# Performance work log

Measured on AMD Instinct MI355X. Metric: run time of the kernel, lower is better.

The kernel has to match this reference:

```python
import jax, jax.numpy as jnp
import numpy as np

B, N, RD = 32, 2000, 32
E, H, A = 128, 256, 8
NUM_ACTIONS = N
ACTION_NORM = float(NUM_ACTIONS)


def _mlp2(x, W1, b1, W2, b2):
    return jnp.maximum(x @ W1 + b1, 0.0) @ W2 + b2


def setup_inputs() -> dict:
    key = jax.random.key(0)
    ks = jax.random.split(key, 8)
    s = lambda fan_in: 1.0 / np.sqrt(fan_in)
    return {
        "state": jax.random.normal(ks[0], (B, N, RD), jnp.float32),
        "distance_matrix": jax.random.uniform(ks[1], (N, N), jnp.float32),
        "W_emb1": jax.random.normal(ks[2], (RD, H), jnp.float32) * s(RD),
        "b_emb1": jnp.zeros((H,), jnp.float32),
        "W_emb2": jax.random.normal(ks[3], (H, E), jnp.float32) * s(H),
        "b_emb2": jnp.zeros((E,), jnp.float32),
        "Wq1": jax.random.normal(ks[4], (E + A, H), jnp.float32) * s(E + A),
        "bq1": jnp.zeros((H,), jnp.float32),
        "Wq2": jax.random.normal(ks[5], (H, 1), jnp.float32) * s(H),
        "bq2": jnp.zeros((1,), jnp.float32),
        "fixed_actions": jax.random.randint(ks[6], (3, B), 0, NUM_ACTIONS, jnp.int32),
        "fixed_agent_ids": jnp.arange(3, dtype=jnp.int32),
    }


def reference(state, distance_matrix, W_emb1, b_emb1, W_emb2, b_emb2,
              Wq1, bq1, Wq2, bq2, fixed_actions, fixed_agent_ids):
    # normalized distance -> similarity, row-stochastic
    dm = distance_matrix / distance_matrix.max()
    sim = jnp.exp(-dm)  # scaling = 1 (use_nn_scaling=False)
    sim = sim / sim.sum(-1, keepdims=True)

    enc = _mlp2(state, W_emb1, b_emb1, W_emb2, b_emb2)      # [B,N,E]
    x = jnp.einsum('nm,bme->bne', sim, enc)                 # graph conv mix

    idx_f = jnp.arange(N, dtype=x.dtype)

    def qnet(actions):
        # actions: [B,A] broadcast over node axis -> concat -> MLP -> [B,N]
        act = jnp.broadcast_to(actions[:, None, :], (B, N, A))
        feat = jnp.concatenate([x, act], axis=-1)           # [B,N,E+A]
        return _mlp2(feat, Wq1, bq1, Wq2, bq2)[..., 0]      # [B,N]

    # init actions: -1 everywhere, fixed agents get given action / norm
    actions = jnp.full((B, A), -1.0, dtype=x.dtype)
    actions = actions.at[:, fixed_agent_ids].set(
        fixed_actions.T.astype(x.dtype) / ACTION_NORM)

    # sequential per-agent soft-argmax loop (second torch loop; the first
    # torch loop's q-values are fully overwritten here, so it is dead code)
    q_cols = []
    for agent_id in range(A):
        q = qnet(actions)                                   # [B,N]
        sam = jnp.clip(jax.nn.softmax(q, axis=-1) @ idx_f, 0.0, float(NUM_ACTIONS))
        actions = actions.at[:, agent_id].set(
            jax.lax.stop_gradient(sam / ACTION_NORM))
        q2 = qnet(actions)
        qv = jnp.take_along_axis(q2, sam.astype(jnp.int32)[:, None], axis=-1)[:, 0]
        q_cols.append(qv)

    q_values = jnp.stack(q_cols, axis=1)                    # [B,A]
    chosen = (actions * ACTION_NORM).astype(jnp.int32)      # [B,A]
    return q_values, chosen
```

## Files before the change

### kernel.cpp

```cpp
#include <hip/hip_runtime.h>
#include <cstddef>

#define NB 32
#define NN 2000
#define NRD 32
#define NE 128
#define NH 256
#define NA 8
#define KP8 2048
#define NGP 128
#define H1S 264
#define XT8S 136
#define ACTION_NORM 2000.0f

typedef unsigned short u16;
typedef unsigned char u8;
typedef __bf16 b16x8 __attribute__((ext_vector_type(8)));
typedef float f32x4 __attribute__((ext_vector_type(4)));
typedef const __attribute__((address_space(1))) unsigned int* gptr_t;
typedef __attribute__((address_space(3))) unsigned int* lptr_t;

__device__ inline u16 f2bf(float x) {
    unsigned u = __float_as_uint(x);
    u += 0x7FFFu + ((u >> 16) & 1u);
    return (u16)(u >> 16);
}
__device__ inline float bf2f(u16 h) { return __uint_as_float((unsigned)h << 16); }
__device__ inline u8 f2fp8(float x) {
    return (u8)(__builtin_amdgcn_cvt_pk_fp8_f32(x, x, 0, false) & 0xFF);
}
__device__ inline u16 f2fp8x2(float a, float b) {
    return (u16)(__builtin_amdgcn_cvt_pk_fp8_f32(a, b, 0, false) & 0xFFFF);
}
__device__ inline float fp82f(u8 b) {
    return __builtin_amdgcn_cvt_pk_f32_fp8((unsigned)b, false)[0];
}
__device__ inline int kswz(int m) {
    return (m & ~63) + (((m >> 3) & 3) << 4) + (((m >> 5) & 1) << 3) + (m & 7);
}

#define PREP_STATE (64000 * 32)
#define PREP_W1T   (256 * 32)
#define PREP_W2T   (128 * 256)
#define PREP_WQ1T  (256 * 128)
#define PREP_PAD   (4096 * 48)
#define PREP_TOT   (PREP_STATE + PREP_W1T + PREP_W2T + PREP_WQ1T + PREP_PAD)
#define PREP_BLOCKS (PREP_TOT / 256)
#define MAX_BLOCKS 1024
__global__ __launch_bounds__(256) void k_front(
        const float* __restrict__ state, const float* __restrict__ W1,
        const float* __restrict__ W2, const float* __restrict__ Wq1,
        const float* __restrict__ dm, const int* __restrict__ fa,
        const int* __restrict__ fid,
        u16* __restrict__ state_b, u16* __restrict__ W1t,
        u16* __restrict__ W2t, u8* __restrict__ Wq1f8,
        u8* __restrict__ encb, float* __restrict__ pmax,
        float* __restrict__ actions, float* __restrict__ ap0,
        float2* __restrict__ part0) {
    __shared__ float sh[256];
    const int blk = blockIdx.x, t = threadIdx.x;
    if (blk < PREP_BLOCKS) {
        int i = blk * 256 + t;
        if (i < PREP_STATE) { state_b[i] = f2bf(state[i]); return; }
        i -= PREP_STATE;
        if (i < PREP_W1T) { int h = i >> 5, k = i & 31; W1t[i] = f2bf(W1[k * NH + h]); return; }
        i -= PREP_W1T;
        if (i < PREP_W2T) { int e = i >> 8, h = i & 255; W2t[i] = f2bf(W2[h * NE + e]); return; }
        i -= PREP_W2T;
        if (i < PREP_WQ1T) { int hq = i >> 7, e = i & 127; Wq1f8[i] = f2fp8(Wq1[e * NH + hq]); return; }
        i -= PREP_WQ1T;
        if (i < PREP_PAD) { int eb = i / 48, mm = NN + (i % 48); encb[(size_t)eb * KP8 + kswz(mm)] = 0; }
        return;
    }
    if (blk < PREP_BLOCKS + MAX_BLOCKS) {
        const int bid = blk - PREP_BLOCKS;
        float m = 0.0f;
        for (size_t i = (size_t)bid * 256 + t; i < (size_t)NN * NN; i += (size_t)MAX_BLOCKS * 256)
            m = fmaxf(m, dm[i]);
        sh[t] = m; __syncthreads();
        for (int s = 128; s > 0; s >>= 1) {
            if (t < s) sh[t] = fmaxf(sh[t], sh[t + s]);
            __syncthreads();
        }
        if (t == 0) pmax[bid] = sh[0];
        return;
    }
    const int b = t >> 3, a = t & 7;
    float v = -1.0f;
    for (int j = 0; j < 3; ++j)
        if (fid[j] == a) v = (float)fa[j * NB + b] / ACTION_NORM;
    actions[t] = v;
    sh[t] = v;
    __syncthreads();
    float wq[NA];
#pragma unroll
    for (int aa = 0; aa < NA; ++aa) wq[aa] = Wq1[(size_t)(NE + aa) * NH + t];
    for (int bb = 0; bb < NB; ++bb) {
        float s = 0.0f;
#pragma unroll
        for (int aa = 0; aa < NA; ++aa) s = fmaf(sh[bb * NA + aa], wq[aa], s);
        ap0[bb * NH + t] = s;
    }
    for (int i = t; i < NB * NGP; i += 256) part0[i] = make_float2(0.0f, 0.0f);
}

__global__ __launch_bounds__(512) void k_sim(
        const float* __restrict__ dm, const float* __restrict__ pmax,
        u8* __restrict__ simb, float* __restrict__ inv_rs) {
    __shared__ float shf[512];
    __shared__ u8 srow[KP8];
    const int n = blockIdx.x, t = threadIdx.x;
    float m = fmaxf(pmax[t], pmax[t + 512]);
    shf[t] = m; __syncthreads();
    for (int s = 256; s > 0; s >>= 1) {
        if (t < s) shf[t] = fmaxf(shf[t], shf[t + s]);
        __syncthreads();
    }
    const float inv = 1.0f / shf[0];
    __syncthreads();
    float s = 0.0f;
    for (int mm = t * 2; mm < KP8; mm += 1024) {
        float e0 = 0.0f, e1 = 0.0f;
        if (mm < NN)     { e0 = expf(-dm[(size_t)n * NN + mm] * inv);     s += e0; }
        if (mm + 1 < NN) { e1 = expf(-dm[(size_t)n * NN + mm + 1] * inv); s += e1; }
        *(u16*)(srow + kswz(mm)) = f2fp8x2(e0, e1);
    }
    shf[t] = s; __syncthreads();
    for (int st = 256; st > 0; st >>= 1) {
        if (t < st) shf[t] += shf[t + st];
        __syncthreads();
    }
    if (t == 0) inv_rs[n] = 1.0f / shf[0];
    if (t < 128) *(uint4*)(simb + (size_t)n * KP8 + t * 16) = *(const uint4*)(srow + t * 16);
}

__global__ __launch_bounds__(512) void k_enc(
        const u16* __restrict__ state_b, const u16* __restrict__ W1t,
        const u16* __restrict__ W2t, u8* __restrict__ encb,
        const float* __restrict__ b1, const float* __restrict__ b2) {
    __shared__ u16 stage[20 * 512];
    __shared__ u16 h1t[64 * H1S];
    const int blk = blockIdx.x, tid = threadIdx.x;
    const int w = tid >> 6, l = tid & 63;
    const int lm = l & 15, lq = l >> 4;
    const int gm = blk * 64;

    {
#pragma unroll
        for (int i = 0; i < 3; ++i) {
            const int idx = w * 3 + i;
            if (idx < 20) {
                const u16* gp;
                if (idx < 4) gp = state_b + (size_t)(gm + idx * 16 + lm) * NRD + lq * 8;
                else         gp = W1t + (size_t)((idx - 4) * 16 + lm) * NRD + lq * 8;
                __builtin_amdgcn_global_load_lds((gptr_t)gp, (lptr_t)(stage + idx * 512), 16, 0, 0);
            }
        }
        __syncthreads();
        b16x8 af[4], bf[2];
#pragma unroll
        for (int i = 0; i < 4; ++i) af[i] = *(const b16x8*)(stage + i * 512 + l * 8);
#pragma unroll
        for (int j = 0; j < 2; ++j) bf[j] = *(const b16x8*)(stage + (4 + w * 2 + j) * 512 + l * 8);
        f32x4 acc1[4][2] = {};
#pragma unroll
        for (int i = 0; i < 4; ++i)
#pragma unroll
            for (int j = 0; j < 2; ++j)
                acc1[i][j] = __builtin_amdgcn_mfma_f32_16x16x32_bf16(af[i], bf[j], acc1[i][j], 0, 0, 0);
#pragma unroll
        for (int i = 0; i < 4; ++i)
#pragma unroll
            for (int r = 0; r < 4; ++r) {
                const int row = i * 16 + lq * 4 + r;
#pragma unroll
                for (int j = 0; j < 2; ++j) {
                    const int col = w * 32 + j * 16 + lm;
                    h1t[row * H1S + col] = f2bf(fmaxf(acc1[i][j][r] + b1[col], 0.0f));
                }
            }
    }

    const int wr = w & 3, wc = w >> 2;
    f32x4 acc2[2][2] = {};
    const u16* gpw = W2t + (size_t)(w * 16 + lm) * NH + lq * 8;
    __syncthreads();
    __builtin_amdgcn_global_load_lds((gptr_t)gpw, (lptr_t)(stage + w * 512), 16, 0, 0);
    __syncthreads();
    for (int t = 0; t < 8; ++t) {
        const int cur = t & 1;
        if (t < 7) {
            gpw += 32;
            __builtin_amdgcn_global_load_lds((gptr_t)gpw,
                (lptr_t)(stage + (cur ^ 1) * 4096 + w * 512), 16, 0, 0);
        }
        const u16* base = stage + cur * 4096;
        b16x8 af2[2], bf2[2];
#pragma unroll
        for (int i = 0; i < 2; ++i)
            af2[i] = *(const b16x8*)(base + (wr * 2 + i) * 512 + l * 8);
#pragma unroll
        for (int j = 0; j < 2; ++j)
            bf2[j] = *(const b16x8*)(h1t + (wc * 32 + j * 16 + lm) * H1S + t * 32 + lq * 8);
#pragma unroll
        for (int i = 0; i < 2; ++i)
#pragma unroll
            for (int j = 0; j < 2; ++j)
                acc2[i][j] = __builtin_amdgcn_mfma_f32_16x16x32_bf16(af2[i], bf2[j], acc2[i][j], 0, 0, 0);
        __syncthreads();
    }

    u8* etile = (u8*)stage;
#pragma unroll
    for (int i = 0; i < 2; ++i)
#pragma unroll
        for (int r = 0; r < 4; ++r) {
            const int e = wr * 32 + i * 16 + lq * 4 + r;
            const float bias = b2[e];
#pragma unroll
            for (int j = 0; j < 2; ++j) {
                const int off = wc * 32 + j * 16 + lm;
                etile[e * 64 + off] = f2fp8(acc2[i][j][r] + bias);
            }
        }
    __syncthreads();
#pragma unroll
    for (int u0 = 0; u0 < 2; ++u0) {
        const int u = u0 * 512 + tid;
        const int e = u >> 3, run = u & 7;
        const int rg0 = gm + run * 8;
        const unsigned bb = (unsigned)rg0 / 2000u;
        const unsigned m0 = (unsigned)rg0 - bb * 2000u;
        const int wbyte = (int)(m0 & ~63u) + (int)(((m0 >> 3) & 3u) << 4) + (int)(((m0 >> 5) & 1u) << 3);
        const uint2 v = *(const uint2*)(etile + e * 64 + run * 8);
        *(uint2*)(encb + ((size_t)bb * 128 + e) * KP8 + wbyte) = v;
    }
}

__global__ __launch_bounds__(512) void k_conv_y0(
        const u8* __restrict__ simb, const u8* __restrict__ encb,
        const u8* __restrict__ Wq1f8, const float* __restrict__ inv_rs,
        const float* __restrict__ bq1, const float* __restrict__ ap0,
        const float* __restrict__ Wq2, u8* __restrict__ y0f8,
        float2* __restrict__ part0) {
    __shared__ u8 lds[3 * 16384];
    __shared__ float qsum[64 * 8];
    const int tid = threadIdx.x;
    const int w = tid >> 6, l = tid & 63;
    const int wr = w & 1, wc = w >> 1;
    const int L = blockIdx.x + (int)(blockIdx.y << 4);
    const int g = L & 7, ii = L >> 3;
    const int bx = (g & 1) * 8 + (ii & 7);
    const int by = (g >> 1) * 8 + (ii >> 3);
    const int bm = bx * 128;
    const int bb = by;
    const int lm = l & 15, lq = l >> 4;
    const u8* Bt = encb + (size_t)bb * 128 * KP8;
    typedef long lx2 __attribute__((ext_vector_type(2)));

    f32x4 acc[4][2] = {};

    const u8* gpt[2];
#pragma unroll
    for (int i = 0; i < 2; ++i) {
        const int idx = w * 2 + i;
        if (idx < 8) {
            int row = bm + idx * 16 + lm;
            row = row < NN ? row : NN - 1;
            gpt[i] = simb + (size_t)row * KP8 + lq * 16;
        } else {
            gpt[i] = Bt + (size_t)((idx - 8) * 16 + lm) * KP8 + lq * 16;
        }
    }

    auto STAGE = [&](int kt, int buf) {
#pragma unroll
        for (int i = 0; i < 2; ++i)
            __builtin_amdgcn_global_load_lds((gptr_t)(gpt[i] + kt * 64),
                (lptr_t)(lds + buf * 16384 + (w * 2 + i) * 1024), 16, 0, 0);
    };
    auto COMPUTE = [&](int buf) {
        const u8* curb = lds + buf * 16384;
        const int fo = l * 16;
        lx2 af[4], bf[2];
#pragma unroll
        for (int i = 0; i < 4; ++i)
            af[i] = *(const lx2*)(curb + (wr * 4 + i) * 1024 + fo);
#pragma unroll
        for (int j = 0; j < 2; ++j)
            bf[j] = *(const lx2*)(curb + (8 + wc * 2 + j) * 1024 + fo);
        __builtin_amdgcn_s_setprio(1);
#pragma unroll
        for (int i = 0; i < 4; ++i)
#pragma unroll
            for (int j = 0; j < 2; ++j) {
                acc[i][j] = __builtin_amdgcn_mfma_f32_16x16x32_fp8_fp8(af[i][0], bf[j][0], acc[i][j], 0, 0, 0);
                acc[i][j] = __builtin_amdgcn_mfma_f32_16x16x32_fp8_fp8(af[i][1], bf[j][1], acc[i][j], 0, 0, 0);
            }
        __builtin_amdgcn_s_setprio(0);
    };

#define FENCE() __builtin_amdgcn_sched_barrier(0)
#define WAIT_VM(N) do { FENCE(); asm volatile("s_waitcnt vmcnt(" #N ")" ::: "memory"); FENCE(); } while (0)
#define BARRIER() do { FENCE(); __builtin_amdgcn_s_barrier(); FENCE(); } while (0)

    STAGE(0, 0);
    STAGE(1, 1);
    WAIT_VM(2); BARRIER();
    for (int t = 0; t < 30; ++t) {
        STAGE(t + 2, (t + 2) % 3);
        COMPUTE(t % 3);
        WAIT_VM(2); BARRIER();
    }
    COMPUTE(0);
    WAIT_VM(0); BARRIER();
    COMPUTE(1);
    BARRIER();
#undef WAIT_VM
#undef BARRIER
#undef FENCE

#pragma unroll
    for (int i = 0; i < 4; ++i) {
#pragma unroll
        for (int r = 0; r < 4; ++r) {
            const int row = wr * 64 + i * 16 + lq * 4 + r;
            const int gn = bm + row;
            const float rsv = inv_rs[gn < NN ? gn : NN - 1];
#pragma unroll
            for (int j = 0; j < 2; ++j) {
                const int col = wc * 32 + j * 16 + lm;
                lds[row * XT8S + col] = f2fp8(acc[i][j][r] * rsv);
            }
        }
    }
    __syncthreads();

    const int h0 = w * 32;
    float bq1v[2], apv[2], w2vv[2];
#pragma unroll
    for (int j = 0; j < 2; ++j) {
        const int h = h0 + j * 16 + lm;
        bq1v[j] = bq1[h];
        apv[j] = ap0[bb * NH + h];
        w2vv[j] = Wq2[h];
    }
    float se_tot = 0.0f, sn_tot = 0.0f;

    for (int half = 0; half < 2; ++half) {
        f32x4 acc2[4][2] = {};
#pragma unroll
        for (int ks = 0; ks < 4; ++ks) {
            long bfw[2];
#pragma unroll
            for (int j = 0; j < 2; ++j)
                bfw[j] = *(const long*)(Wq1f8 + (size_t)(h0 + j * 16 + lm) * NE + ks * 32 + lq * 8);
#pragma unroll
            for (int i = 0; i < 4; ++i) {
                const long afx = *(const long*)(lds + (half * 64 + i * 16 + lm) * XT8S + ks * 32 + lq * 8);
#pragma unroll
                for (int j = 0; j < 2; ++j)
                    acc2[i][j] = __builtin_amdgcn_mfma_f32_16x16x32_fp8_fp8(afx, bfw[j], acc2[i][j], 0, 0, 0);
            }
        }
#pragma unroll
        for (int i = 0; i < 4; ++i) {
#pragma unroll
            for (int r = 0; r < 4; ++r) {
                const int rl = i * 16 + lq * 4 + r;
                const int n = bm + half * 64 + rl;
                float q = 0.0f;
#pragma unroll
                for (int j = 0; j < 2; ++j) {
                    const float v = acc2[i][j][r] + bq1v[j];
                    if (n < NN) y0f8[((size_t)n * NB + bb) * NH + h0 + j * 16 + lm] = f2fp8(v);
                    q += fmaxf(v + apv[j], 0.0f) * w2vv[j];
                }
#pragma unroll
                for (int off = 1; off < 16; off <<= 1) q += __shfl_xor(q, off);
                if (lm == 0) qsum[rl * 8 + w] = q;
            }
        }
        __syncthreads();
        if (tid < 64) {
            const int n = bm + half * 64 + tid;
            float q = 0.0f;
#pragma unroll
            for (int wv = 0; wv < 8; ++wv) q += qsum[tid * 8 + wv];
            float e = (n < NN) ? expf(fminf(q, 60.0f)) : 0.0f;
            float sne = e * (float)n;
#pragma unroll
            for (int off = 32; off > 0; off >>= 1) {
                e += __shfl_xor(e, off); sne += __shfl_xor(sne, off);
            }
            if (tid == 0) { se_tot += e; sn_tot += sne; }
        }
        __syncthreads();
    }
    if (tid == 0) part0[bb * NGP + bx] = make_float2(se_tot, sn_tot);
}

__global__ __launch_bounds__(256) void k_agent(
        const u8* __restrict__ y0f8, const float* __restrict__ Wq1,
        const float* __restrict__ Wq2, const float* __restrict__ bq2,
        float* actions, const int* __restrict__ fa, const int* __restrict__ fid,
        const float* __restrict__ apb, float* __restrict__ apbase_out,
        const float2* __restrict__ pin, float2* __restrict__ pout,
        float* __restrict__ out, int ag) {
    __shared__ float sh[256];
    __shared__ float s_sam;
    const int t = threadIdx.x;
    const int lane = t & 63, wave = t >> 6;
    const int wg = blockIdx.x * 4 + wave;
    const int b = wg & 31, ng = wg >> 5;
    const int hl = lane & 15, qtr = lane >> 4;
    const int idx = ag - 1;

    uint4 yv[4];
#pragma unroll
    for (int k = 0; k < 4; ++k) {
        const int n = 4 * (ng + k * NGP) + qtr;
        yv[k] = *(const uint4*)(y0f8 + (((size_t)n * NB + b) << 8) + hl * 16);
    }

    float samn;
    {
        const float2 p0 = pin[b * NGP + lane];
        const float2 p1 = pin[b * NGP + 64 + lane];
        float se0 = p0.x + p1.x, sn0 = p0.y + p1.y;
#pragma unroll
        for (int m = 32; m > 0; m >>= 1) {
            se0 += __shfl_xor(se0, m); sn0 += __shfl_xor(sn0, m);
        }
        const float sam = fminf(fmaxf(sn0 / se0, 0.0f), 2000.0f);
        samn = sam * (1.0f / ACTION_NORM);
    }
    float iv = -1.0f;
    for (int j = 0; j < 3; ++j)
        if (fid[j] == idx) iv = (float)fa[j * NB + b] * (1.0f / ACTION_NORM);
    const float d = samn - iv;

    float ap16[16], w2v[16];
    {
        const float4* ab  = (const float4*)(apb + b * NH + hl * 16);
        const float4* wq  = (const float4*)(Wq1 + (size_t)(NE + idx) * NH + hl * 16);
        const float4* w2p = (const float4*)(Wq2 + hl * 16);
#pragma unroll
        for (int jj = 0; jj < 4; ++jj) {
            const float4 a4 = ab[jj]; const float4 w4 = wq[jj]; const float4 v4 = w2p[jj];
            ap16[jj * 4 + 0] = fmaf(d, w4.x, a4.x);
            ap16[jj * 4 + 1] = fmaf(d, w4.y, a4.y);
            ap16[jj * 4 + 2] = fmaf(d, w4.z, a4.z);
            ap16[jj * 4 + 3] = fmaf(d, w4.w, a4.w);
            w2v[jj * 4 + 0] = v4.x; w2v[jj * 4 + 1] = v4.y;
            w2v[jj * 4 + 2] = v4.z; w2v[jj * 4 + 3] = v4.w;
        }
    }

    float se = 0.0f, sn = 0.0f;
#pragma unroll
    for (int k = 0; k < 4; ++k) {
        const int n = 4 * (ng + k * NGP) + qtr;
        const unsigned dw[4] = {yv[k].x, yv[k].y, yv[k].z, yv[k].w};
        float q = 0.0f;
#pragma unroll
        for (int dd = 0; dd < 4; ++dd) {
            const auto lo = __builtin_amdgcn_cvt_pk_f32_fp8(dw[dd], false);
            const auto hi = __builtin_amdgcn_cvt_pk_f32_fp8(dw[dd], true);
            q += fmaxf(lo[0] + ap16[dd * 4 + 0], 0.f) * w2v[dd * 4 + 0];
            q += fmaxf(lo[1] + ap16[dd * 4 + 1], 0.f) * w2v[dd * 4 + 1];
            q += fmaxf(hi[0] + ap16[dd * 4 + 2], 0.f) * w2v[dd * 4 + 2];
            q += fmaxf(hi[1] + ap16[dd * 4 + 3], 0.f) * w2v[dd * 4 + 3];
        }
#pragma unroll
        for (int off = 1; off < 16; off <<= 1) q += __shfl_xor(q, off);
        if (n < NN) {
            const float e = expf(fminf(q, 60.0f));
            se += e; sn += e * (float)n;
        }
    }
    se += __shfl_xor(se, 16); sn += __shfl_xor(sn, 16);
    se += __shfl_xor(se, 32); sn += __shfl_xor(sn, 32);
    if (lane == 0) pout[b * NGP + ng] = make_float2(se, sn);

    if (blockIdx.x < NB) {
        const int bb = blockIdx.x;
        if (wave == 0) {
            const float2 p0 = pin[bb * NGP + lane];
            const float2 p1 = pin[bb * NGP + 64 + lane];
            float a1 = p0.x + p1.x, a2 = p0.y + p1.y;
#pragma unroll
            for (int m = 32; m > 0; m >>= 1) {
                a1 += __shfl_xor(a1, m); a2 += __shfl_xor(a2, m);
            }
            if (lane == 0) s_sam = fminf(fmaxf(a2 / a1, 0.0f), 2000.0f);
        }
        __syncthreads();
        const float sam = s_sam;
        const float samf = sam * (1.0f / ACTION_NORM);
        float apt = 0.0f;
#pragma unroll
        for (int a = 0; a < NA; ++a) {
            const float av = (a == idx) ? samf : actions[bb * NA + a];
            apt = fmaf(av, Wq1[(size_t)(NE + a) * NH + t], apt);
        }
        apbase_out[bb * NH + t] = apt;
        int nsel = (int)sam; if (nsel > NN - 1) nsel = NN - 1;
        const float yv2 = fp82f(y0f8[((size_t)nsel * NB + bb) * NH + t]);
        sh[t] = fmaxf(yv2 + apt, 0.0f) * Wq2[t];
        __syncthreads();
        for (int s = 128; s > 0; s >>= 1) {
            if (t < s) sh[t] += sh[t + s];
            __syncthreads();
        }
        if (t == 0) {
            out[bb * NA + idx] = sh[0] + bq2[0];
            actions[bb * NA + idx] = samf;
        }
    }
}

__global__ __launch_bounds__(256) void k_fin(
        const u8* __restrict__ y0f8, const float* __restrict__ Wq1,
        const float* __restrict__ Wq2, const float* __restrict__ bq2,
        const float* __restrict__ actions, const float2* __restrict__ pin,
        float* __restrict__ out) {
    __shared__ float sh[256];
    __shared__ float s_sam;
    const int bb = blockIdx.x, t = threadIdx.x;
    const int lane = t & 63, wave = t >> 6;
    if (wave == 0) {
        const float2 p0 = pin[bb * NGP + lane];
        const float2 p1 = pin[bb * NGP + 64 + lane];
        float a1 = p0.x + p1.x, a2 = p0.y + p1.y;
#pragma unroll
        for (int m = 32; m > 0; m >>= 1) {
            a1 += __shfl_xor(a1, m); a2 += __shfl_xor(a2, m);
        }
        if (lane == 0) s_sam = fminf(fmaxf(a2 / a1, 0.0f), 2000.0f);
    }
    __syncthreads();
    const float sam = s_sam;
    const float samn = sam * (1.0f / ACTION_NORM);
    float apt = 0.0f;
#pragma unroll
    for (int a = 0; a < NA; ++a) {
        const float av = (a == NA - 1) ? samn : actions[bb * NA + a];
        apt = fmaf(av, Wq1[(size_t)(NE + a) * NH + t], apt);
    }
    int nsel = (int)sam; if (nsel > NN - 1) nsel = NN - 1;
    const float yv = fp82f(y0f8[((size_t)nsel * NB + bb) * NH + t]);
    sh[t] = fmaxf(yv + apt, 0.0f) * Wq2[t];
    __syncthreads();
    for (int s = 128; s > 0; s >>= 1) {
        if (t < s) sh[t] += sh[t + s];
        __syncthreads();
    }
    if (t == 0) out[bb * NA + (NA - 1)] = sh[0] + bq2[0];
    if (t < NA) {
        const float av = (t == NA - 1) ? samn : actions[bb * NA + t];
        out[NB * NA + bb * NA + t] = (float)(int)(av * ACTION_NORM);
    }
}

extern "C" void kernel_launch(void* const* d_in, const int* in_sizes, int n_in,
                              void* d_out, int out_size, void* d_ws, size_t ws_size,
                              hipStream_t stream) {
    const float* state = (const float*)d_in[0];
    const float* dm    = (const float*)d_in[1];
    const float* W1    = (const float*)d_in[2];
    const float* b1    = (const float*)d_in[3];
    const float* W2    = (const float*)d_in[4];
    const float* b2    = (const float*)d_in[5];
    const float* Wq1   = (const float*)d_in[6];
    const float* bq1   = (const float*)d_in[7];
    const float* Wq2   = (const float*)d_in[8];
    const float* bq2   = (const float*)d_in[9];
    const int* fa      = (const int*)d_in[10];
    const int* fid     = (const int*)d_in[11];
    float* out = (float*)d_out;

    char* p = (char*)d_ws;
    u8* simb       = (u8*)p;       p += (size_t)NN * KP8;
    u8* encb       = (u8*)p;       p += (size_t)4096 * KP8;
    float* inv_rs  = (float*)p;    p += 2048 * 4;
    float* pmax    = (float*)p;    p += 1024 * 4;
    float* actions = (float*)p;    p += 256 * 4;
    float* ap0     = (float*)p;    p += 8192 * 4;
    float* apbA    = (float*)p;    p += 8192 * 4;
    float* apbB    = (float*)p;    p += 8192 * 4;
    float2* part0  = (float2*)p;   p += (size_t)NB * NGP * 8;
    float2* part1  = (float2*)p;   p += (size_t)NB * NGP * 8;
    u16* state_b   = (u16*)p;      p += (size_t)2048000 * 2;
    u16* W1t       = (u16*)p;      p += 8192 * 2;
    u16* W2t       = (u16*)p;      p += 32768 * 2;
    u8* Wq1f8      = (u8*)p;       p += 32768;
    u8* y0f8       = (u8*)p;       p += (size_t)2048 * NB * NH;

    k_front<<<PREP_BLOCKS + MAX_BLOCKS + 1, 256, 0, stream>>>(
        state, W1, W2, Wq1, dm, fa, fid,
        state_b, W1t, W2t, Wq1f8, encb, pmax, actions, ap0, part0);
    k_sim<<<NN, 512, 0, stream>>>(dm, pmax, simb, inv_rs);
    k_enc<<<1000, 512, 0, stream>>>(state_b, W1t, W2t, encb, b1, b2);
    k_conv_y0<<<dim3(16, 32), 512, 0, stream>>>(simb, encb, Wq1f8, inv_rs, bq1,
                                                ap0, Wq2, y0f8, part0);
    for (int ag = 1; ag < NA; ++ag) {
        const float2* pin  = (ag & 1) ? part0 : part1;
        float2*       pout = (ag & 1) ? part1 : part0;
        const float*  apb  = (ag == 1) ? ap0 : ((ag & 1) ? apbB : apbA);
        float*        apo  = (ag & 1) ? apbA : apbB;
        k_agent<<<1024, 256, 0, stream>>>(y0f8, Wq1, Wq2, bq2, actions,
                                          fa, fid, apb, apo,
                                          pin, pout, out, ag);
    }
    k_fin<<<NB, 256, 0, stream>>>(y0f8, Wq1, Wq2, bq2, actions, part1, out);
}
```

Measured before the change: 223.3 us.

## Merge sim and encoder kernels, halve conv tile rows to double grid

The similarity-row kernel and the encoder MLP kernel are merged into one launch, with block index selecting the role, so the two independent stages run concurrently and one launch is saved. The graph-conv kernel tile shrinks from 128 to 64 node rows, doubling the grid to 1024 blocks for better CU occupancy on a small problem. Only 6 of 8 waves now issue loads, and each block's partial softmax sums cover 64 nodes. The smaller tile lowers per-block reuse of the encoder operand, and the merged kernel carries the encoder's LDS footprint into the sim blocks.

```diff
diff --git a/kernel.cpp b/kernel.cpp
--- a/kernel.cpp
+++ b/kernel.cpp
@@ -104,43 +104,45 @@
     for (int i = t; i < NB * NGP; i += 256) part0[i] = make_float2(0.0f, 0.0f);
 }
 
-__global__ __launch_bounds__(512) void k_sim(
+__global__ __launch_bounds__(512) void k_sim_enc(
+        const u16* __restrict__ state_b, const u16* __restrict__ W1t,
+        const u16* __restrict__ W2t, u8* __restrict__ encb,
+        const float* __restrict__ b1, const float* __restrict__ b2,
         const float* __restrict__ dm, const float* __restrict__ pmax,
         u8* __restrict__ simb, float* __restrict__ inv_rs) {
-    __shared__ float shf[512];
-    __shared__ u8 srow[KP8];
-    const int n = blockIdx.x, t = threadIdx.x;
-    float m = fmaxf(pmax[t], pmax[t + 512]);
-    shf[t] = m; __syncthreads();
-    for (int s = 256; s > 0; s >>= 1) {
-        if (t < s) shf[t] = fmaxf(shf[t], shf[t + s]);
-        __syncthreads();
-    }
-    const float inv = 1.0f / shf[0];
-    __syncthreads();
-    float s = 0.0f;
-    for (int mm = t * 2; mm < KP8; mm += 1024) {
-        float e0 = 0.0f, e1 = 0.0f;
-        if (mm < NN)     { e0 = expf(-dm[(size_t)n * NN + mm] * inv);     s += e0; }
-        if (mm + 1 < NN) { e1 = expf(-dm[(size_t)n * NN + mm + 1] * inv); s += e1; }
-        *(u16*)(srow + kswz(mm)) = f2fp8x2(e0, e1);
-    }
-    shf[t] = s; __syncthreads();
-    for (int st = 256; st > 0; st >>= 1) {
-        if (t < st) shf[t] += shf[t + st];
-        __syncthreads();
-    }
-    if (t == 0) inv_rs[n] = 1.0f / shf[0];
-    if (t < 128) *(uint4*)(simb + (size_t)n * KP8 + t * 16) = *(const uint4*)(srow + t * 16);
-}
-
-__global__ __launch_bounds__(512) void k_enc(
-        const u16* __restrict__ state_b, const u16* __restrict__ W1t,
-        const u16* __restrict__ W2t, u8* __restrict__ encb,
-        const float* __restrict__ b1, const float* __restrict__ b2) {
     __shared__ u16 stage[20 * 512];
     __shared__ u16 h1t[64 * H1S];
     const int blk = blockIdx.x, tid = threadIdx.x;
+
+    if (blk >= 1000) {
+        float* shf = (float*)stage;
+        u8* srow = (u8*)(stage + 1024);
+        const int n = blk - 1000, t = tid;
+        float m = fmaxf(pmax[t], pmax[t + 512]);
+        shf[t] = m; __syncthreads();
+        for (int s = 256; s > 0; s >>= 1) {
+            if (t < s) shf[t] = fmaxf(shf[t], shf[t + s]);
+            __syncthreads();
+        }
+        const float inv = 1.0f / shf[0];
+        __syncthreads();
+        float s = 0.0f;
+        for (int mm = t * 2; mm < KP8; mm += 1024) {
+            float e0 = 0.0f, e1 = 0.0f;
+            if (mm < NN)     { e0 = expf(-dm[(size_t)n * NN + mm] * inv);     s += e0; }
+            if (mm + 1 < NN) { e1 = expf(-dm[(size_t)n * NN + mm + 1] * inv); s += e1; }
+            *(u16*)(srow + kswz(mm)) = f2fp8x2(e0, e1);
+        }
+        shf[t] = s; __syncthreads();
+        for (int st = 256; st > 0; st >>= 1) {
+            if (t < st) shf[t] += shf[t + st];
+            __syncthreads();
+        }
+        if (t == 0) inv_rs[n] = 1.0f / shf[0];
+        if (t < 128) *(uint4*)(simb + (size_t)n * KP8 + t * 16) = *(const uint4*)(srow + t * 16);
+        return;
+    }
+
     const int w = tid >> 6, l = tid & 63;
     const int lm = l & 15, lq = l >> 4;
     const int gm = blk * 64;
@@ -243,55 +245,58 @@
         const float* __restrict__ bq1, const float* __restrict__ ap0,
         const float* __restrict__ Wq2, u8* __restrict__ y0f8,
         float2* __restrict__ part0) {
-    __shared__ u8 lds[3 * 16384];
+    __shared__ u8 lds[3 * 12288];
     __shared__ float qsum[64 * 8];
     const int tid = threadIdx.x;
     const int w = tid >> 6, l = tid & 63;
     const int wr = w & 1, wc = w >> 1;
-    const int L = blockIdx.x + (int)(blockIdx.y << 4);
+    const int L = blockIdx.x + (int)(blockIdx.y << 5);
     const int g = L & 7, ii = L >> 3;
-    const int bx = (g & 1) * 8 + (ii & 7);
-    const int by = (g >> 1) * 8 + (ii >> 3);
-    const int bm = bx * 128;
+    const int bx = (g & 1) * 16 + (ii & 15);
+    const int by = (g >> 1) * 8 + (ii >> 4);
+    const int bm = bx * 64;
     const int bb = by;
     const int lm = l & 15, lq = l >> 4;
     const u8* Bt = encb + (size_t)bb * 128 * KP8;
     typedef long lx2 __attribute__((ext_vector_type(2)));
 
-    f32x4 acc[4][2] = {};
+    f32x4 acc[2][2] = {};
 
     const u8* gpt[2];
 #pragma unroll
     for (int i = 0; i < 2; ++i) {
-        const int idx = w * 2 + i;
-        if (idx < 8) {
-            int row = bm + idx * 16 + lm;
+        const int u = w * 2 + i;
+        if (u < 4) {
+            int row = bm + u * 16 + lm;
             row = row < NN ? row : NN - 1;
             gpt[i] = simb + (size_t)row * KP8 + lq * 16;
         } else {
-            gpt[i] = Bt + (size_t)((idx - 8) * 16 + lm) * KP8 + lq * 16;
+            const int uu = (u < 12) ? u : 11;
+            gpt[i] = Bt + (size_t)((uu - 4) * 16 + lm) * KP8 + lq * 16;
         }
     }
 
     auto STAGE = [&](int kt, int buf) {
-#pragma unroll
-        for (int i = 0; i < 2; ++i)
-            __builtin_amdgcn_global_load_lds((gptr_t)(gpt[i] + kt * 64),
-                (lptr_t)(lds + buf * 16384 + (w * 2 + i) * 1024), 16, 0, 0);
+        if (w < 6) {
+#pragma unroll
+            for (int i = 0; i < 2; ++i)
+                __builtin_amdgcn_global_load_lds((gptr_t)(gpt[i] + kt * 64),
+                    (lptr_t)(lds + buf * 12288 + (w * 2 + i) * 1024), 16, 0, 0);
+        }
     };
     auto COMPUTE = [&](int buf) {
-        const u8* curb = lds + buf * 16384;
+        const u8* curb = lds + buf * 12288;
         const int fo = l * 16;
-        lx2 af[4], bf[2];
-#pragma unroll
-        for (int i = 0; i < 4; ++i)
-            af[i] = *(const lx2*)(curb + (wr * 4 + i) * 1024 + fo);
+        lx2 af[2], bf[2];
+#pragma unroll
+        for (int i = 0; i < 2; ++i)
+            af[i] = *(const lx2*)(curb + (wr * 2 + i) * 1024 + fo);
 #pragma unroll
         for (int j = 0; j < 2; ++j)
-            bf[j] = *(const lx2*)(curb + (8 + wc * 2 + j) * 1024 + fo);
+            bf[j] = *(const lx2*)(curb + 4096 + (wc * 2 + j) * 1024 + fo);
         __builtin_amdgcn_s_setprio(1);
 #pragma unroll
-        for (int i = 0; i < 4; ++i)
+        for (int i = 0; i < 2; ++i)
 #pragma unroll
             for (int j = 0; j < 2; ++j) {
                 acc[i][j] = __builtin_amdgcn_mfma_f32_16x16x32_fp8_fp8(af[i][0], bf[j][0], acc[i][j], 0, 0, 0);
@@ -321,10 +326,10 @@
 #undef FENCE
 
 #pragma unroll
-    for (int i = 0; i < 4; ++i) {
+    for (int i = 0; i < 2; ++i) {
 #pragma unroll
         for (int r = 0; r < 4; ++r) {
-            const int row = wr * 64 + i * 16 + lq * 4 + r;
+            const int row = wr * 32 + i * 16 + lq * 4 + r;
             const int gn = bm + row;
             const float rsv = inv_rs[gn < NN ? gn : NN - 1];
 #pragma unroll
@@ -345,59 +350,54 @@
         apv[j] = ap0[bb * NH + h];
         w2vv[j] = Wq2[h];
     }
-    float se_tot = 0.0f, sn_tot = 0.0f;
-
-    for (int half = 0; half < 2; ++half) {
-        f32x4 acc2[4][2] = {};
-#pragma unroll
-        for (int ks = 0; ks < 4; ++ks) {
-            long bfw[2];
+
+    f32x4 acc2[4][2] = {};
+#pragma unroll
+    for (int ks = 0; ks < 4; ++ks) {
+        long bfw[2];
+#pragma unroll
+        for (int j = 0; j < 2; ++j)
+            bfw[j] = *(const long*)(Wq1f8 + (size_t)(h0 + j * 16 + lm) * NE + ks * 32 + lq * 8);
+#pragma unroll
+        for (int i = 0; i < 4; ++i) {
+            const long afx = *(const long*)(lds + (i * 16 + lm) * XT8S + ks * 32 + lq * 8);
 #pragma unroll
             for (int j = 0; j < 2; ++j)
-                bfw[j] = *(const long*)(Wq1f8 + (size_t)(h0 + j * 16 + lm) * NE + ks * 32 + lq * 8);
-#pragma unroll
-            for (int i = 0; i < 4; ++i) {
-                const long afx = *(const long*)(lds + (half * 64 + i * 16 + lm) * XT8S + ks * 32 + lq * 8);
-#pragma unroll
-                for (int j = 0; j < 2; ++j)
-                    acc2[i][j] = __builtin_amdgcn_mfma_f32_16x16x32_fp8_fp8(afx, bfw[j], acc2[i][j], 0, 0, 0);
+                acc2[i][j] = __builtin_amdgcn_mfma_f32_16x16x32_fp8_fp8(afx, bfw[j], acc2[i][j], 0, 0, 0);
+        }
+    }
+#pragma unroll
+    for (int i = 0; i < 4; ++i) {
+#pragma unroll
+        for (int r = 0; r < 4; ++r) {
+            const int rl = i * 16 + lq * 4 + r;
+            const int n = bm + rl;
+            float q = 0.0f;
+#pragma unroll
+            for (int j = 0; j < 2; ++j) {
+                const float v = acc2[i][j][r] + bq1v[j];
+                if (n < NN) y0f8[((size_t)n * NB + bb) * NH + h0 + j * 16 + lm] = f2fp8(v);
+                q += fmaxf(v + apv[j], 0.0f) * w2vv[j];
             }
-        }
-#pragma unroll
-        for (int i = 0; i < 4; ++i) {
-#pragma unroll
-            for (int r = 0; r < 4; ++r) {
-                const int rl = i * 16 + lq * 4 + r;
-                const int n = bm + half * 64 + rl;
-                float q = 0.0f;
-#pragma unroll
-                for (int j = 0; j < 2; ++j) {
-                    const float v = acc2[i][j][r] + bq1v[j];
-                    if (n < NN) y0f8[((size_t)n * NB + bb) * NH + h0 + j * 16 + lm] = f2fp8(v);
-                    q += fmaxf(v + apv[j], 0.0f) * w2vv[j];
-                }
-#pragma unroll
-                for (int off = 1; off < 16; off <<= 1) q += __shfl_xor(q, off);
-                if (lm == 0) qsum[rl * 8 + w] = q;
-            }
-        }
-        __syncthreads();
-        if (tid < 64) {
-            const int n = bm + half * 64 + tid;
-            float q = 0.0f;
-#pragma unroll
-            for (int wv = 0; wv < 8; ++wv) q += qsum[tid * 8 + wv];
-            float e = (n < NN) ? expf(fminf(q, 60.0f)) : 0.0f;
-            float sne = e * (float)n;
-#pragma unroll
-            for (int off = 32; off > 0; off >>= 1) {
-                e += __shfl_xor(e, off); sne += __shfl_xor(sne, off);
-            }
-            if (tid == 0) { se_tot += e; sn_tot += sne; }
-        }
-        __syncthreads();
-    }
-    if (tid == 0) part0[bb * NGP + bx] = make_float2(se_tot, sn_tot);
+#pragma unroll
+            for (int off = 1; off < 16; off <<= 1) q += __shfl_xor(q, off);
+            if (lm == 0) qsum[rl * 8 + w] = q;
+        }
+    }
+    __syncthreads();
+    if (tid < 64) {
+        const int n = bm + tid;
+        float q = 0.0f;
+#pragma unroll
+        for (int wv = 0; wv < 8; ++wv) q += qsum[tid * 8 + wv];
+        float e = (n < NN) ? expf(fminf(q, 60.0f)) : 0.0f;
+        float sne = e * (float)n;
+#pragma unroll
+        for (int off = 32; off > 0; off >>= 1) {
+            e += __shfl_xor(e, off); sne += __shfl_xor(sne, off);
+        }
+        if (tid == 0) part0[bb * NGP + bx] = make_float2(e, sne);
+    }
 }
 
 __global__ __launch_bounds__(256) void k_agent(
@@ -600,9 +600,9 @@
     k_front<<<PREP_BLOCKS + MAX_BLOCKS + 1, 256, 0, stream>>>(
         state, W1, W2, Wq1, dm, fa, fid,
         state_b, W1t, W2t, Wq1f8, encb, pmax, actions, ap0, part0);
-    k_sim<<<NN, 512, 0, stream>>>(dm, pmax, simb, inv_rs);
-    k_enc<<<1000, 512, 0, stream>>>(state_b, W1t, W2t, encb, b1, b2);
-    k_conv_y0<<<dim3(16, 32), 512, 0, stream>>>(simb, encb, Wq1f8, inv_rs, bq1,
+    k_sim_enc<<<3000, 512, 0, stream>>>(state_b, W1t, W2t, encb, b1, b2,
+                                        dm, pmax, simb, inv_rs);
+    k_conv_y0<<<dim3(32, 32), 512, 0, stream>>>(simb, encb, Wq1f8, inv_rs, bq1,
                                                 ap0, Wq2, y0f8, part0);
     for (int ag = 1; ag < NA; ++ag) {
         const float2* pin  = (ag & 1) ? part0 : part1;
```

Result: slower. 245.8 us (+10.1%).
